# Kernel tuning notes

Measured on AMD Instinct MI355X. Metric: run time of the kernel, lower is better.

## Reference

```python
import jax, jax.numpy as jnp
import numpy as np
import math

HIDDEN_SIZE = 1024  # scale factor uses hidden_size, not D*hidden_size
B, S, H = 32, 2048, 1024  # batch, encoder steps, D*hidden_size (D=1)


def setup_inputs() -> dict:
    key = jax.random.key(0)
    k1, k2 = jax.random.split(key)
    keys = jax.random.normal(k1, (B, S, H), dtype=jnp.float32)
    query = jax.random.normal(k2, (B, H), dtype=jnp.float32)
    return {"keys": keys, "query": query, "t": 0}


def reference(keys, query, t):
    # keys/values: [B, S, H]; query: [B, H]. t is unused by the math (kept for signature parity).
    scale = 1.0 / math.sqrt(HIDDEN_SIZE)
    # attn_scores[b, s] = sum_d query[b, d] * keys[b, s, d] / sqrt(hidden_size)
    scores = jnp.einsum("bd,bsd->bs", query, keys) * scale
    attn = jax.nn.softmax(scores, axis=1)  # over encoder steps
    # attn_values[b, d] = sum_s attn[b, s] * values[b, s, d]  (values == keys)
    attn_values = jnp.einsum("bs,bsd->bd", attn, keys)
    return attn_values, attn[:, :, None]
```

## Files before the change

### kernel.cpp

```cpp
#include <hip/hip_runtime.h>
#include <math.h>

constexpr int B = 32, S = 2048, H = 1024;
constexpr float SCALE = 0.03125f;

constexpr int NC1 = 32;
constexpr int ROWS_PER_BLOCK = S / NC1;
constexpr int ROWS_PER_WAVE  = ROWS_PER_BLOCK / 4;

constexpr int ND4 = 16;

constexpr size_t WS_ML  = 0;
constexpr size_t WS_MLG = WS_ML + (size_t)B * NC1 * 2;

__device__ __forceinline__ float dot4(const float4 a, const float4 q) {
  return a.x * q.x + a.y * q.y + a.z * q.z + a.w * q.w;
}

__global__ __launch_bounds__(256) void k1_scores(
    const float* __restrict__ keys, const float* __restrict__ query,
    float* __restrict__ out_attn, float* __restrict__ ws) {
  const int b = blockIdx.x / NC1;
  const int c = blockIdx.x % NC1;
  const int t = threadIdx.x;
  const int wave = t >> 6, lane = t & 63;
  const int srow0 = c * ROWS_PER_BLOCK + wave * ROWS_PER_WAVE;

  const float* kb = keys + (size_t)b * S * H;
  const float* qb = query + (size_t)b * H;

  const float4 q0 = *(const float4*)(qb + 0 * 256 + lane * 4);
  const float4 q1 = *(const float4*)(qb + 1 * 256 + lane * 4);
  const float4 q2 = *(const float4*)(qb + 2 * 256 + lane * 4);
  const float4 q3 = *(const float4*)(qb + 3 * 256 + lane * 4);

  float m = -INFINITY, l = 0.f;

  for (int s = srow0; s < srow0 + ROWS_PER_WAVE; s += 2) {
    const float* r0 = kb + (size_t)s * H;
    const float* r1 = kb + (size_t)(s + 1) * H;
    const float4 a0 = *(const float4*)(r0 + 0 * 256 + lane * 4);
    const float4 a1 = *(const float4*)(r0 + 1 * 256 + lane * 4);
    const float4 a2 = *(const float4*)(r0 + 2 * 256 + lane * 4);
    const float4 a3 = *(const float4*)(r0 + 3 * 256 + lane * 4);
    const float4 b0 = *(const float4*)(r1 + 0 * 256 + lane * 4);
    const float4 b1 = *(const float4*)(r1 + 1 * 256 + lane * 4);
    const float4 b2 = *(const float4*)(r1 + 2 * 256 + lane * 4);
    const float4 b3 = *(const float4*)(r1 + 3 * 256 + lane * 4);

    float d0 = dot4(a0, q0) + dot4(a1, q1) + dot4(a2, q2) + dot4(a3, q3);
    float d1 = dot4(b0, q0) + dot4(b1, q1) + dot4(b2, q2) + dot4(b3, q3);
#pragma unroll
    for (int off = 1; off < 64; off <<= 1) {
      d0 += __shfl_xor(d0, off);
      d1 += __shfl_xor(d1, off);
    }
    d0 *= SCALE;
    d1 *= SCALE;
    if (lane == 0) {
      out_attn[(size_t)b * S + s]     = d0;
      out_attn[(size_t)b * S + s + 1] = d1;
    }
    const float mn = fmaxf(m, fmaxf(d0, d1));
    l = l * __expf(m - mn) + __expf(d0 - mn) + __expf(d1 - mn);
    m = mn;
  }

  __shared__ float wm[4], wl[4];
  if (lane == 0) { wm[wave] = m; wl[wave] = l; }
  __syncthreads();
  if (t == 0) {
    const float M = fmaxf(fmaxf(wm[0], wm[1]), fmaxf(wm[2], wm[3]));
    const float L = wl[0] * __expf(wm[0] - M) + wl[1] * __expf(wm[1] - M) +
                    wl[2] * __expf(wm[2] - M) + wl[3] * __expf(wm[3] - M);
    float* ml = ws + WS_ML;
    ml[((size_t)b * NC1 + c) * 2 + 0] = M;
    ml[((size_t)b * NC1 + c) * 2 + 1] = L;
  }
}

__global__ __launch_bounds__(64) void k2_merge(float* __restrict__ ws) {
  const int b = blockIdx.x;
  const int lane = threadIdx.x;
  const float* ml = ws + WS_ML;
  float m = -INFINITY, l = 0.f;
  if (lane < NC1) {
    m = ml[((size_t)b * NC1 + lane) * 2 + 0];
    l = ml[((size_t)b * NC1 + lane) * 2 + 1];
  }
  float M = m;
#pragma unroll
  for (int off = 1; off < 64; off <<= 1) M = fmaxf(M, __shfl_xor(M, off));
  float e = l * __expf(m - M);
#pragma unroll
  for (int off = 1; off < 64; off <<= 1) e += __shfl_xor(e, off);
  if (lane == 0) {
    ws[WS_MLG + b * 2 + 0] = M;
    ws[WS_MLG + b * 2 + 1] = e;
  }
}

__global__ __launch_bounds__(256) void k3_weights(
    float* __restrict__ out_attn, const float* __restrict__ ws) {
  const int i = blockIdx.x * 256 + threadIdx.x;
  const int b = i >> 11;
  const float M = ws[WS_MLG + b * 2 + 0];
  const float invL = 1.0f / ws[WS_MLG + b * 2 + 1];
  out_attn[i] = __expf(out_attn[i] - M) * invL;
}

__global__ __launch_bounds__(256) void k4_values(
    const float* __restrict__ keys, const float* __restrict__ attn,
    float* __restrict__ out_values) {
  const int b   = blockIdx.x / ND4;
  const int dsl = blockIdx.x % ND4;
  const int t = threadIdx.x;
  const int r = t >> 6;
  const int cc = t & 63;
  const float* kb = keys + (size_t)b * S * H + (size_t)dsl * 64 + cc;
  const float* ab = attn + (size_t)b * S;

  float acc = 0.f;
  for (int s0 = r; s0 < S; s0 += 64) {
    float kv[16], av[16];
#pragma unroll
    for (int u = 0; u < 16; ++u) {
      const int s = s0 + 4 * u;
      kv[u] = kb[(size_t)s * H];
      av[u] = ab[s];
    }
#pragma unroll
    for (int u = 0; u < 16; ++u) acc = fmaf(av[u], kv[u], acc);
  }

  __shared__ float part[4][64];
  part[r][cc] = acc;
  __syncthreads();
  if (t < 64) {
    const float v = part[0][t] + part[1][t] + part[2][t] + part[3][t];
    out_values[(size_t)b * H + (size_t)dsl * 64 + t] = v;
  }
}

extern "C" void kernel_launch(void* const* d_in, const int* in_sizes, int n_in,
                              void* d_out, int out_size, void* d_ws, size_t ws_size,
                              hipStream_t stream) {
  const float* keys  = (const float*)d_in[0];
  const float* query = (const float*)d_in[1];
  float* out = (float*)d_out;
  float* ws  = (float*)d_ws;

  float* out_values = out;
  float* out_attn   = out + (size_t)B * H;

  k1_scores<<<B * NC1, 256, 0, stream>>>(keys, query, out_attn, ws);
  k2_merge<<<B, 64, 0, stream>>>(ws);
  k3_weights<<<(B * S) / 256, 256, 0, stream>>>(out_attn, ws);
  k4_values<<<B * ND4, 256, 0, stream>>>(keys, out_attn, out_values);
}
```

Baseline: 403.0 us.

## Fuse score and value passes into a single-pass online-softmax split-K kernel

Replaces the separate score pass and value pass over keys with one flash-decoding style kernel. Each block computes scores for a chunk of rows, keeps a running max and sum, and accumulates rescaled partial outputs from the same loaded keys, so keys are read once instead of twice. A combine kernel then merges the per-chunk partial outputs and statistics. The fused path needs a larger workspace for the partial outputs, adds two block barriers per tile of eight rows, and falls back to the old path when the workspace is too small.

```diff
diff --git a/kernel.cpp b/kernel.cpp
--- a/kernel.cpp
+++ b/kernel.cpp
@@ -4,38 +4,158 @@
 constexpr int B = 32, S = 2048, H = 1024;
 constexpr float SCALE = 0.03125f;
 
-constexpr int NC1 = 32;
-constexpr int ROWS_PER_BLOCK = S / NC1;
+constexpr int NC = 32;
+constexpr int SC = S / NC;
+constexpr int TILE = 8;
+
+constexpr size_t WS_ML  = 0;
+constexpr size_t WS_MLG = WS_ML + (size_t)B * NC * 2;
+constexpr size_t WS_O   = WS_MLG + (size_t)B * 2;
+constexpr size_t WS_NEEDED_BYTES = (WS_O + (size_t)B * NC * H) * sizeof(float);
+
+__global__ __launch_bounds__(256) void k1_fused(
+    const float* __restrict__ keys, const float* __restrict__ query,
+    float* __restrict__ out_attn, float* __restrict__ ws) {
+  const int b = blockIdx.x / NC;
+  const int c = blockIdx.x % NC;
+  const int t = threadIdx.x;
+  const int d0 = t * 4;
+  const int wave = t >> 6, lane = t & 63;
+
+  float* ml       = ws + WS_ML;
+  float* o_chunks = ws + WS_O;
+
+  const float* kb = keys + (size_t)b * S * H + (size_t)c * SC * H;
+  const float4 q = *(const float4*)(query + (size_t)b * H + d0);
+
+  float m = -INFINITY, l = 0.0f;
+  float o0 = 0.f, o1 = 0.f, o2 = 0.f, o3 = 0.f;
+
+  __shared__ float red[4][TILE];
+
+  for (int s0 = 0; s0 < SC; s0 += TILE) {
+    float4 k[TILE];
+    float p[TILE];
+#pragma unroll
+    for (int j = 0; j < TILE; ++j) {
+      k[j] = *(const float4*)(kb + (size_t)(s0 + j) * H + d0);
+      p[j] = k[j].x * q.x + k[j].y * q.y + k[j].z * q.z + k[j].w * q.w;
+    }
+#pragma unroll
+    for (int off = 32; off > 0; off >>= 1) {
+#pragma unroll
+      for (int j = 0; j < TILE; ++j) p[j] += __shfl_down(p[j], off);
+    }
+    if (lane == 0) {
+#pragma unroll
+      for (int j = 0; j < TILE; ++j) red[wave][j] = p[j];
+    }
+    __syncthreads();
+    float snew[TILE];
+    float mt = m;
+#pragma unroll
+    for (int j = 0; j < TILE; ++j) {
+      snew[j] = (red[0][j] + red[1][j] + red[2][j] + red[3][j]) * SCALE;
+      mt = fmaxf(mt, snew[j]);
+    }
+    if (t < TILE) out_attn[(size_t)b * S + c * SC + s0 + t] = snew[t];
+
+    const float alpha = __expf(m - mt);
+    float w[TILE];
+    float lsum = 0.f;
+#pragma unroll
+    for (int j = 0; j < TILE; ++j) { w[j] = __expf(snew[j] - mt); lsum += w[j]; }
+    l = l * alpha + lsum;
+    o0 *= alpha; o1 *= alpha; o2 *= alpha; o3 *= alpha;
+#pragma unroll
+    for (int j = 0; j < TILE; ++j) {
+      o0 += w[j] * k[j].x;
+      o1 += w[j] * k[j].y;
+      o2 += w[j] * k[j].z;
+      o3 += w[j] * k[j].w;
+    }
+    m = mt;
+    __syncthreads();
+  }
+
+  *(float4*)(o_chunks + ((size_t)b * NC + c) * H + d0) =
+      make_float4(o0, o1, o2, o3);
+  if (t == 0) {
+    ml[((size_t)b * NC + c) * 2 + 0] = m;
+    ml[((size_t)b * NC + c) * 2 + 1] = l;
+  }
+}
+
+__global__ __launch_bounds__(256) void k2_combine(
+    float* __restrict__ ws, float* __restrict__ out_values) {
+  const int b = blockIdx.x;
+  const int t = threadIdx.x;
+  const int d0 = t * 4;
+
+  const float* ml       = ws + WS_ML;
+  const float* o_chunks = ws + WS_O;
+
+  float M = -INFINITY;
+#pragma unroll 4
+  for (int c = 0; c < NC; ++c)
+    M = fmaxf(M, ml[((size_t)b * NC + c) * 2 + 0]);
+  float L = 0.f;
+#pragma unroll 4
+  for (int c = 0; c < NC; ++c) {
+    const float mc = ml[((size_t)b * NC + c) * 2 + 0];
+    const float lc = ml[((size_t)b * NC + c) * 2 + 1];
+    L += lc * __expf(mc - M);
+  }
+  float a0 = 0.f, a1 = 0.f, a2 = 0.f, a3 = 0.f;
+  for (int c = 0; c < NC; ++c) {
+    const float mc = ml[((size_t)b * NC + c) * 2 + 0];
+    const float wgt = __expf(mc - M);
+    const float4 oc = *(const float4*)(o_chunks + ((size_t)b * NC + c) * H + d0);
+    a0 += wgt * oc.x; a1 += wgt * oc.y; a2 += wgt * oc.z; a3 += wgt * oc.w;
+  }
+  const float inv = 1.0f / L;
+  *(float4*)(out_values + (size_t)b * H + d0) =
+      make_float4(a0 * inv, a1 * inv, a2 * inv, a3 * inv);
+  if (t == 0) {
+    ws[WS_MLG + b * 2 + 0] = M;
+    ws[WS_MLG + b * 2 + 1] = L;
+  }
+}
+
+__global__ __launch_bounds__(256) void k3_norm(
+    float* __restrict__ out_attn, const float* __restrict__ ws) {
+  const int i = blockIdx.x * 256 + threadIdx.x;
+  const int b = i >> 11;
+  const float M = ws[WS_MLG + b * 2 + 0];
+  const float invL = 1.0f / ws[WS_MLG + b * 2 + 1];
+  out_attn[i] = __expf(out_attn[i] - M) * invL;
+}
+
+constexpr int ROWS_PER_BLOCK = SC;
 constexpr int ROWS_PER_WAVE  = ROWS_PER_BLOCK / 4;
-
 constexpr int ND4 = 16;
-
-constexpr size_t WS_ML  = 0;
-constexpr size_t WS_MLG = WS_ML + (size_t)B * NC1 * 2;
 
 __device__ __forceinline__ float dot4(const float4 a, const float4 q) {
   return a.x * q.x + a.y * q.y + a.z * q.z + a.w * q.w;
 }
 
-__global__ __launch_bounds__(256) void k1_scores(
+__global__ __launch_bounds__(256) void k1b_scores(
     const float* __restrict__ keys, const float* __restrict__ query,
     float* __restrict__ out_attn, float* __restrict__ ws) {
-  const int b = blockIdx.x / NC1;
-  const int c = blockIdx.x % NC1;
+  const int b = blockIdx.x / NC;
+  const int c = blockIdx.x % NC;
   const int t = threadIdx.x;
   const int wave = t >> 6, lane = t & 63;
   const int srow0 = c * ROWS_PER_BLOCK + wave * ROWS_PER_WAVE;
 
   const float* kb = keys + (size_t)b * S * H;
   const float* qb = query + (size_t)b * H;
-
   const float4 q0 = *(const float4*)(qb + 0 * 256 + lane * 4);
   const float4 q1 = *(const float4*)(qb + 1 * 256 + lane * 4);
   const float4 q2 = *(const float4*)(qb + 2 * 256 + lane * 4);
   const float4 q3 = *(const float4*)(qb + 3 * 256 + lane * 4);
 
   float m = -INFINITY, l = 0.f;
-
   for (int s = srow0; s < srow0 + ROWS_PER_WAVE; s += 2) {
     const float* r0 = kb + (size_t)s * H;
     const float* r1 = kb + (size_t)(s + 1) * H;
@@ -47,7 +167,6 @@
     const float4 b1 = *(const float4*)(r1 + 1 * 256 + lane * 4);
     const float4 b2 = *(const float4*)(r1 + 2 * 256 + lane * 4);
     const float4 b3 = *(const float4*)(r1 + 3 * 256 + lane * 4);
-
     float d0 = dot4(a0, q0) + dot4(a1, q1) + dot4(a2, q2) + dot4(a3, q3);
     float d1 = dot4(b0, q0) + dot4(b1, q1) + dot4(b2, q2) + dot4(b3, q3);
 #pragma unroll
@@ -55,8 +174,7 @@
       d0 += __shfl_xor(d0, off);
       d1 += __shfl_xor(d1, off);
     }
-    d0 *= SCALE;
-    d1 *= SCALE;
+    d0 *= SCALE; d1 *= SCALE;
     if (lane == 0) {
       out_attn[(size_t)b * S + s]     = d0;
       out_attn[(size_t)b * S + s + 1] = d1;
@@ -65,7 +183,6 @@
     l = l * __expf(m - mn) + __expf(d0 - mn) + __expf(d1 - mn);
     m = mn;
   }
-
   __shared__ float wm[4], wl[4];
   if (lane == 0) { wm[wave] = m; wl[wave] = l; }
   __syncthreads();
@@ -73,20 +190,18 @@
     const float M = fmaxf(fmaxf(wm[0], wm[1]), fmaxf(wm[2], wm[3]));
     const float L = wl[0] * __expf(wm[0] - M) + wl[1] * __expf(wm[1] - M) +
                     wl[2] * __expf(wm[2] - M) + wl[3] * __expf(wm[3] - M);
-    float* ml = ws + WS_ML;
-    ml[((size_t)b * NC1 + c) * 2 + 0] = M;
-    ml[((size_t)b * NC1 + c) * 2 + 1] = L;
-  }
-}
-
-__global__ __launch_bounds__(64) void k2_merge(float* __restrict__ ws) {
+    ws[WS_ML + ((size_t)b * NC + c) * 2 + 0] = M;
+    ws[WS_ML + ((size_t)b * NC + c) * 2 + 1] = L;
+  }
+}
+
+__global__ __launch_bounds__(64) void k2b_merge(float* __restrict__ ws) {
   const int b = blockIdx.x;
   const int lane = threadIdx.x;
-  const float* ml = ws + WS_ML;
   float m = -INFINITY, l = 0.f;
-  if (lane < NC1) {
-    m = ml[((size_t)b * NC1 + lane) * 2 + 0];
-    l = ml[((size_t)b * NC1 + lane) * 2 + 1];
+  if (lane < NC) {
+    m = ws[WS_ML + ((size_t)b * NC + lane) * 2 + 0];
+    l = ws[WS_ML + ((size_t)b * NC + lane) * 2 + 1];
   }
   float M = m;
 #pragma unroll
@@ -100,16 +215,7 @@
   }
 }
 
-__global__ __launch_bounds__(256) void k3_weights(
-    float* __restrict__ out_attn, const float* __restrict__ ws) {
-  const int i = blockIdx.x * 256 + threadIdx.x;
-  const int b = i >> 11;
-  const float M = ws[WS_MLG + b * 2 + 0];
-  const float invL = 1.0f / ws[WS_MLG + b * 2 + 1];
-  out_attn[i] = __expf(out_attn[i] - M) * invL;
-}
-
-__global__ __launch_bounds__(256) void k4_values(
+__global__ __launch_bounds__(256) void k4b_values(
     const float* __restrict__ keys, const float* __restrict__ attn,
     float* __restrict__ out_values) {
   const int b   = blockIdx.x / ND4;
@@ -119,7 +225,6 @@
   const int cc = t & 63;
   const float* kb = keys + (size_t)b * S * H + (size_t)dsl * 64 + cc;
   const float* ab = attn + (size_t)b * S;
-
   float acc = 0.f;
   for (int s0 = r; s0 < S; s0 += 64) {
     float kv[16], av[16];
@@ -132,13 +237,12 @@
 #pragma unroll
     for (int u = 0; u < 16; ++u) acc = fmaf(av[u], kv[u], acc);
   }
-
   __shared__ float part[4][64];
   part[r][cc] = acc;
   __syncthreads();
   if (t < 64) {
-    const float v = part[0][t] + part[1][t] + part[2][t] + part[3][t];
-    out_values[(size_t)b * H + (size_t)dsl * 64 + t] = v;
+    out_values[(size_t)b * H + (size_t)dsl * 64 + t] =
+        part[0][t] + part[1][t] + part[2][t] + part[3][t];
   }
 }
 
@@ -153,8 +257,14 @@
   float* out_values = out;
   float* out_attn   = out + (size_t)B * H;
 
-  k1_scores<<<B * NC1, 256, 0, stream>>>(keys, query, out_attn, ws);
-  k2_merge<<<B, 64, 0, stream>>>(ws);
-  k3_weights<<<(B * S) / 256, 256, 0, stream>>>(out_attn, ws);
-  k4_values<<<B * ND4, 256, 0, stream>>>(keys, out_attn, out_values);
-}
+  if (ws_size >= WS_NEEDED_BYTES) {
+    k1_fused<<<B * NC, 256, 0, stream>>>(keys, query, out_attn, ws);
+    k2_combine<<<B, 256, 0, stream>>>(ws, out_values);
+    k3_norm<<<(B * S) / 256, 256, 0, stream>>>(out_attn, ws);
+  } else {
+    k1b_scores<<<B * NC, 256, 0, stream>>>(keys, query, out_attn, ws);
+    k2b_merge<<<B, 64, 0, stream>>>(ws);
+    k3_norm<<<(B * S) / 256, 256, 0, stream>>>(out_attn, ws);
+    k4b_values<<<B * ND4, 256, 0, stream>>>(keys, out_attn, out_values);
+  }
+}
```

Result: faster. 369.8 us (-8.2%).
